# Kernel tuning notes

Measured on AMD Instinct MI355X. Metric: run time of the kernel, lower is better.

Reference implementation:

```python
import jax, jax.numpy as jnp
import numpy as np
from jax import lax

B, T_PAST, T_FUT, F_IN, F_OUT, H = 512, 128, 48, 64, 16, 512


def setup_inputs() -> dict:
    key = jax.random.key(0)
    ks = jax.random.split(key, 12)
    s = jnp.float32(0.05)
    p = lambda k, shape: jax.random.normal(k, shape, jnp.float32) * s
    return {
        "inp": jax.random.normal(ks[0], (B, T_PAST, F_IN), jnp.float32),
        "target_seq": jax.random.normal(ks[1], (B, T_FUT, F_OUT), jnp.float32),
        "enc1_Wk": p(ks[2], (F_IN, 4 * H)), "enc1_Wr": p(ks[3], (H, 4 * H)), "enc1_b": jnp.zeros((4 * H,), jnp.float32),
        "enc2_Wk": p(ks[4], (H, 4 * H)), "enc2_Wr": p(ks[5], (H, 4 * H)), "enc2_b": jnp.zeros((4 * H,), jnp.float32),
        "dec1_Wk": p(ks[6], (F_OUT, 4 * H)), "dec1_Wr": p(ks[7], (H, 4 * H)), "dec1_b": jnp.zeros((4 * H,), jnp.float32),
        "dec2_Wk": p(ks[8], (H, 4 * H)), "dec2_Wr": p(ks[9], (H, 4 * H)), "dec2_b": jnp.zeros((4 * H,), jnp.float32),
        "fc_W": p(ks[10], (H, F_OUT)), "fc_b": jnp.zeros((F_OUT,), jnp.float32),
    }


def _gates(z, c_prev):
    # Keras gate order: i, f, g(cell), o
    i, f, g, o = jnp.split(z, 4, axis=-1)
    c = jax.nn.sigmoid(f) * c_prev + jax.nn.sigmoid(i) * jnp.tanh(g)
    h = jax.nn.sigmoid(o) * jnp.tanh(c)
    return h, c


def _lstm_layer(xs, h0, c0, Wk, Wr, b):
    # xs: (B, T, D) -> (hs (B,T,H), hT, cT)
    xz = jnp.einsum("btd,dg->btg", xs, Wk) + b  # input projection precomputed
    def step(carry, xz_t):
        h, c = carry
        h2, c2 = _gates(xz_t + h @ Wr, c)
        return (h2, c2), h2
    (hT, cT), hs = lax.scan(step, (h0, c0), jnp.swapaxes(xz, 0, 1))
    return jnp.swapaxes(hs, 0, 1), hT, cT


def reference(inp, target_seq,
              enc1_Wk, enc1_Wr, enc1_b, enc2_Wk, enc2_Wr, enc2_b,
              dec1_Wk, dec1_Wr, dec1_b, dec2_Wk, dec2_Wr, dec2_b,
              fc_W, fc_b):
    b = inp.shape[0]
    z = jnp.zeros((b, H), inp.dtype)
    # Encoder: layer2 initial state = layer1 final state (as in source)
    h1s, h1, c1 = _lstm_layer(inp, z, z, enc1_Wk, enc1_Wr, enc1_b)
    _, h2, c2 = _lstm_layer(h1s, h1, c1, enc2_Wk, enc2_Wr, enc2_b)
    # Decoder: every future step restarts from (h2, c2) with teacher-forced
    # inputs -> steps are independent, compute all in parallel.
    z1 = (jnp.einsum("btf,fg->btg", target_seq, dec1_Wk)
          + (h2 @ dec1_Wr)[:, None, :] + dec1_b)          # (B, Tf, 4H)
    h1d, c1d = _gates(z1, c2[:, None, :])
    # layer2: input = h1d, initial state = (h1d, c1d) (chained per source)
    z2 = jnp.einsum("bth,hg->btg", h1d, dec2_Wk + dec2_Wr) + dec2_b
    h2d, _ = _gates(z2, c1d)
    return jnp.einsum("bth,hf->btf", h2d, fc_W) + fc_b    # (B, Tf, F_OUT)
```

## Files before the change

### kernel.cpp

```cpp
#include <hip/hip_runtime.h>


typedef _Float16 f16;
typedef _Float16 h8 __attribute__((ext_vector_type(8)));
typedef _Float16 h4 __attribute__((ext_vector_type(4)));
typedef float f32x4 __attribute__((ext_vector_type(4)));
typedef unsigned long long ull;

#define DEV static __device__ __forceinline__

constexpr int NB   = 512;
constexpr int TP   = 128;
constexpr int TFU  = 48;
constexpr int FIN  = 64;
constexpr int FOUT = 16;
constexpr int HS   = 512;
constexpr int G4   = 2048;

DEV float sigf(float x) { return 1.0f / (1.0f + __expf(-x)); }
DEV float tanh_(float x) { float e = __expf(2.0f * x); return 1.0f - 2.0f / (e + 1.0f); }

DEV void issue_ld(h8& d, const f16* p) {
  asm volatile("global_load_dwordx4 %0, %1, off" : "=v"(d) : "v"(p));
}
DEV void issue_ldc(h8& d, const f16* p) {
  asm volatile("global_load_dwordx4 %0, %1, off sc0 sc1" : "=v"(d) : "v"(p));
}
#define ILDX(dst, base, B) \
  asm volatile("global_load_dwordx4 %0, %1, off offset:" #B : "=v"(dst) : "v"(base));
#define ASM_VM0    asm volatile("s_waitcnt vmcnt(0)" ::: "memory")
#define ASM_VMC(N) asm volatile("s_waitcnt vmcnt(" #N ")" ::: "memory")
#define SBAR       __builtin_amdgcn_sched_barrier(0)

DEV void st_coh_h4(f16* p, h4 v) {
  union { h4 h; ull u; } c;
  c.h = v;
  __hip_atomic_store((ull*)p, c.u, __ATOMIC_RELAXED, __HIP_MEMORY_SCOPE_AGENT);
}

DEV unsigned xcc_id() {
  unsigned x;
  asm("s_getreg_b32 %0, hwreg(HW_REG_XCC_ID)" : "=s"(x));
  return x & 7;
}

DEV int ic2zc(int ic) { return ((ic >> 4) & 3) * 512 + ((ic >> 6) << 4) + (ic & 15); }

__global__ void k_conv(const float* __restrict__ a, const float* __restrict__ b,
                       f16* __restrict__ a16, f16* __restrict__ b16) {
  const size_t NA = (size_t)NB * TP * FIN;
  const size_t NBT = (size_t)NB * TFU * FOUT;
  for (size_t i = (size_t)blockIdx.x * blockDim.x + threadIdx.x; i < NA + NBT;
       i += (size_t)gridDim.x * blockDim.x) {
    if (i < NA) a16[i] = (f16)a[i];
    else        b16[i - NA] = (f16)b[i - NA];
  }
}

__global__ void k_bias(const float* __restrict__ b1, const float* __restrict__ b2,
                       const float* __restrict__ b3, const float* __restrict__ b4,
                       float* __restrict__ o1, float* __restrict__ o2,
                       float* __restrict__ o3, float* __restrict__ o4) {
  int ic = blockIdx.x * blockDim.x + threadIdx.x;
  if (ic < G4) {
    int zc = ic2zc(ic);
    o1[ic] = b1[zc]; o2[ic] = b2[zc]; o3[ic] = b3[zc]; o4[ic] = b4[zc];
  }
}

__global__ void k_pack(const float* __restrict__ A, const float* __restrict__ Bs,
                       int split, int NKC, int mode, f16* __restrict__ dst) {
  int i = blockIdx.x * blockDim.x + threadIdx.x;
  int total = 128 * NKC * 64;
  if (i >= total) return;
  int lane = i & 63, rem = i >> 6;
  int kc = rem % NKC, nt = rem / NKC;
  int zc = ic2zc(nt * 16 + (lane & 15));
  int k0 = kc * 32 + ((lane >> 4) << 3);
  h8 v;
#pragma unroll
  for (int j = 0; j < 8; j++) {
    int k = k0 + j;
    float x;
    if (mode == 2) x = A[(size_t)k * G4 + zc] + Bs[(size_t)k * G4 + zc];
    else x = (k < split) ? A[(size_t)k * G4 + zc] : Bs[(size_t)(k - split) * G4 + zc];
    v[j] = (f16)x;
  }
  *(h8*)(dst + (size_t)i * 8) = v;
}

__global__ void k_pack_dk16(const float* __restrict__ W, f16* __restrict__ dst) {
  int i = blockIdx.x * blockDim.x + threadIdx.x;
  if (i >= 128 * 64) return;
  int lane = i & 63, nt = i >> 6;
  int zc = ic2zc(nt * 16 + (lane & 15));
  h4 v;
#pragma unroll
  for (int j = 0; j < 4; j++) v[j] = (f16)W[(size_t)(((lane >> 4) << 2) + j) * G4 + zc];
  *(h4*)(dst + (size_t)i * 4) = v;
}

__global__ void k_pack_fc(const float* __restrict__ W, f16* __restrict__ dst) {
  int i = blockIdx.x * blockDim.x + threadIdx.x;
  if (i >= 32 * 64) return;
  int lane = i & 63, q = i >> 6;
  h4 v;
#pragma unroll
  for (int j = 0; j < 4; j++) {
    int k = q * 16 + ((lane >> 4) << 2) + j;
    v[j] = (f16)W[(size_t)k * FOUT + (lane & 15)];
  }
  *(h4*)(dst + (size_t)i * 4) = v;
}

template <int L, bool HIST>
__global__ __launch_bounds__(256, 1) void k_enc(
    const f16* __restrict__ wfrag, const float* __restrict__ biasI,
    f16* __restrict__ h1s, f16* __restrict__ h2r, f16* __restrict__ h2s,
    float* __restrict__ cT, const float* __restrict__ cInit,
    const f16* __restrict__ inp16, unsigned int* __restrict__ flags,
    int* __restrict__ roster) {
  constexpr int XKC = (L == 1) ? 2 : 16;
  constexpr int NKC = XKC + 16;
  constexpr size_t SLOT = (size_t)NB * HS;
  constexpr bool PLAIN_H = (L == 1) || HIST;

  extern __shared__ __align__(16) char smem[];
  f16* Bl = (f16*)smem;
  float* zl = (float*)(smem + (size_t)NKC * 4096);
  __shared__ int s_gc[2];

  const int tid = threadIdx.x, lane = tid & 63, wid = tid >> 6;
  const int wr = wid & 1, wc = wid >> 1;

  if (tid == 0) {
    unsigned x = xcc_id();
    int slot = atomicAdd(&roster[x], 1) & 31;
    s_gc[0] = (int)x; s_gc[1] = slot;
  }
  __syncthreads();
  const int g = s_gc[0], c = s_gc[1];
  const int b0 = g * 64;
  const int l15 = lane & 15, lk = (lane >> 4) << 3;
  const int trow = tid >> 2, tcol = (tid & 3) << 2;
  const int fbase = g * 32;

  const int kc0 = ((c >> 1) + 1) & 15;
  ull m1 = 0;
  for (int i = 0; i < 8; i++) m1 |= (3ull << (2 * ((kc0 + i) & 15)));
  const ull m2 = 0xFFFFFFFFull & ~m1;

  {
    const uint4* src = (const uint4*)wfrag + (size_t)c * NKC * 256;
    uint4* dst = (uint4*)smem;
    for (int i = tid; i < NKC * 256; i += 256) dst[i] = src[i];
  }

  float bs[4][4];
#pragma unroll
  for (int ga = 0; ga < 4; ga++) {
    f32x4 bv = *(const f32x4*)(biasI + 64 * c + 16 * ga + tcol);
#pragma unroll
    for (int jj = 0; jj < 4; jj++) bs[ga][jj] = bv[jj];
  }

  float cst[4];
  if (L == 1) {
    cst[0] = cst[1] = cst[2] = cst[3] = 0.0f;
  } else {
    f32x4 cv = *(const f32x4*)(cInit + (size_t)(b0 + trow) * HS + 16 * c + tcol);
#pragma unroll
    for (int jj = 0; jj < 4; jj++) cst[jj] = cv[jj];
  }

  int arow[2];
#pragma unroll
  for (int m = 0; m < 2; m++) arow[m] = b0 + 32 * wr + 16 * m + l15;

  const f16* bbase[2];
#pragma unroll
  for (int n = 0; n < 2; n++) bbase[n] = Bl + ((size_t)(2 * wc + n) * NKC * 64 + lane) * 8;
  const f16* bh0 = bbase[0] + (size_t)XKC * 512;
  const f16* bh1 = bbase[1] + (size_t)XKC * 512;

  const size_t aoff0 = ((size_t)(lk >> 4) * 512 + arow[0]) * 16 + (lk & 8);
  const size_t aoff1 = ((size_t)(lk >> 4) * 512 + arow[1]) * 16 + (lk & 8);

  __syncthreads();

#define POLLW(MASK)                                                            \
  {                                                                            \
    const unsigned int tgt = (unsigned int)t;                                  \
    for (;;) {                                                                 \
      unsigned int v = __hip_atomic_load(                                      \
          &flags[(size_t)(fbase + (lane & 31)) * 16], __ATOMIC_RELAXED,        \
          __HIP_MEMORY_SCOPE_AGENT);                                           \
      ull b = __ballot((int)(v >= tgt));                                       \
      if ((b & (MASK)) == (MASK)) break;                                       \
      __builtin_amdgcn_s_sleep(1);                                             \
    }                                                                          \
    SBAR;                                                                      \
  }

  for (int t = 0; t < TP; t++) {
    h8 ax0[XKC], ax1[XKC];
    if (L == 1) {
      const f16* xb0 = inp16 + ((size_t)arow[0] * TP + t) * FIN + lk;
      const f16* xb1 = inp16 + ((size_t)arow[1] * TP + t) * FIN + lk;
      ILDX(ax0[0], xb0, 0) ILDX(ax0[1], xb0, 64)
      ILDX(ax1[0], xb1, 0) ILDX(ax1[1], xb1, 64)
    } else {
      const f16* xb = h1s + (size_t)(t + 1) * SLOT;
      const f16* xp0 = xb + aoff0;
      const f16* xp1 = xb + aoff1;
#pragma unroll
      for (int kc = 0; kc < XKC; kc++) {
        issue_ld(ax0[kc], xp0);
        issue_ld(ax1[kc], xp1);
        xp0 += 16384; xp1 += 16384;
      }
    }

    if (t > 0) POLLW(m1);
    ASM_VM0; SBAR;

    const f16* hb;
    if (L == 1) hb = h1s + (size_t)t * SLOT;
    else if (HIST) hb = (t == 0) ? (h1s + (size_t)TP * SLOT) : (h2s + (size_t)(t - 1) * SLOT);
    else hb = (t == 0) ? (h1s + (size_t)TP * SLOT) : (h2r + (size_t)((t - 1) & 1) * SLOT);
    const f16* hpb0 = hb + aoff0;
    const f16* hpb1 = hb + aoff1;

    h8 hA0[4], hA1[4], hB0[4], hB1[4];
#define LD_H(D, P) { if constexpr (PLAIN_H) issue_ld(D, P); else issue_ldc(D, P); }
#define HB_ISSUE(B0, B1, P)                                                    \
  {                                                                            \
    _Pragma("unroll") for (int j = 0; j < 4; j++) {                            \
      int kk = (kc0 + (P) + j) & 15;                                           \
      const f16* q0 = hpb0 + (size_t)kk * 16384;                               \
      const f16* q1 = hpb1 + (size_t)kk * 16384;                               \
      LD_H(B0[j], q0)                                                          \
      LD_H(B1[j], q1)                                                          \
    }                                                                          \
  }
#define HB_MFMA(B0, B1, P)                                                     \
  {                                                                            \
    _Pragma("unroll") for (int j = 0; j < 4; j++) {                            \
      int kk = (kc0 + (P) + j) & 15;                                           \
      h8 bb0 = *(const h8*)(bh0 + (size_t)kk * 512);                           \
      h8 bb1 = *(const h8*)(bh1 + (size_t)kk * 512);                           \
      acc[0][0] = __builtin_amdgcn_mfma_f32_16x16x32_f16(B0[j], bb0, acc[0][0], 0, 0, 0); \
      acc[0][1] = __builtin_amdgcn_mfma_f32_16x16x32_f16(B0[j], bb1, acc[0][1], 0, 0, 0); \
      acc[1][0] = __builtin_amdgcn_mfma_f32_16x16x32_f16(B1[j], bb0, acc[1][0], 0, 0, 0); \
      acc[1][1] = __builtin_amdgcn_mfma_f32_16x16x32_f16(B1[j], bb1, acc[1][1], 0, 0, 0); \
    }                                                                          \
  }

    HB_ISSUE(hA0, hA1, 0)
    HB_ISSUE(hB0, hB1, 4)

    f32x4 acc[2][2] = {};

#pragma unroll
    for (int kc = 0; kc < XKC; kc++) {
      h8 bb0 = *(const h8*)(bbase[0] + (size_t)kc * 512);
      h8 bb1 = *(const h8*)(bbase[1] + (size_t)kc * 512);
      acc[0][0] = __builtin_amdgcn_mfma_f32_16x16x32_f16(ax0[kc], bb0, acc[0][0], 0, 0, 0);
      acc[0][1] = __builtin_amdgcn_mfma_f32_16x16x32_f16(ax0[kc], bb1, acc[0][1], 0, 0, 0);
      acc[1][0] = __builtin_amdgcn_mfma_f32_16x16x32_f16(ax1[kc], bb0, acc[1][0], 0, 0, 0);
      acc[1][1] = __builtin_amdgcn_mfma_f32_16x16x32_f16(ax1[kc], bb1, acc[1][1], 0, 0, 0);
    }

    ASM_VMC(8); SBAR;
    HB_MFMA(hA0, hA1, 0)
    if (t > 0) POLLW(m2);
    HB_ISSUE(hA0, hA1, 8)
    ASM_VMC(8); SBAR;
    HB_MFMA(hB0, hB1, 4)
    HB_ISSUE(hB0, hB1, 12)
    ASM_VMC(8); SBAR;
    HB_MFMA(hA0, hA1, 8)
    ASM_VMC(0); SBAR;
    HB_MFMA(hB0, hB1, 12)
#undef HB_ISSUE
#undef HB_MFMA
#undef LD_H

#pragma unroll
    for (int m = 0; m < 2; m++)
#pragma unroll
      for (int n = 0; n < 2; n++) {
        int zr = 32 * wr + 16 * m + ((lane >> 4) << 2);
        int zc_ = 32 * wc + 16 * n + l15;
#pragma unroll
        for (int r = 0; r < 4; r++) zl[(size_t)(zr + r) * 68 + zc_] = acc[m][n][r];
      }
    __syncthreads();

    h4 hv;
    {
      const float* zrow = zl + (size_t)trow * 68 + tcol;
      f32x4 z0 = *(const f32x4*)(zrow + 0);
      f32x4 z1 = *(const f32x4*)(zrow + 16);
      f32x4 z2 = *(const f32x4*)(zrow + 32);
      f32x4 z3 = *(const f32x4*)(zrow + 48);
#pragma unroll
      for (int jj = 0; jj < 4; jj++) {
        float zi = z0[jj] + bs[0][jj];
        float zf = z1[jj] + bs[1][jj];
        float zg = z2[jj] + bs[2][jj];
        float zo = z3[jj] + bs[3][jj];
        float ci = sigf(zf) * cst[jj] + sigf(zi) * tanh_(zg);
        cst[jj] = ci;
        hv[jj] = (f16)(sigf(zo) * tanh_(ci));
      }
    }
    {
      f16* hsl;
      if (L == 1) hsl = h1s + (size_t)(t + 1) * SLOT;
      else if (HIST) hsl = h2s + (size_t)t * SLOT;
      else hsl = h2r + (size_t)(t & 1) * SLOT;
      f16* hp = hsl + ((size_t)c * 512 + b0 + trow) * 16 + tcol;
      if constexpr (PLAIN_H) *(h4*)hp = hv;
      else st_coh_h4(hp, hv);
    }
    if (t == TP - 1) {
      f32x4 cp;
#pragma unroll
      for (int jj = 0; jj < 4; jj++) cp[jj] = cst[jj];
      *(f32x4*)(cT + (size_t)(b0 + trow) * HS + 16 * c + tcol) = cp;
    }

    ASM_VM0;
    __syncthreads();
    if (tid == 0)
      __hip_atomic_store(&flags[(size_t)(fbase + c) * 16], (unsigned int)(t + 1),
                         __ATOMIC_RELAXED, __HIP_MEMORY_SCOPE_AGENT);
  }
#undef POLLW
}

__global__ __launch_bounds__(256) void k_d1(const f16* __restrict__ h2T,
                                            const f16* __restrict__ wF,
                                            const float* __restrict__ bI,
                                            float* __restrict__ u) {
  const int tid = threadIdx.x, lane = tid & 63, wid = tid >> 6;
  const int wr = wid & 1, wc = wid >> 1;
  const int r0 = (blockIdx.x >> 4) * 32, ic0 = (blockIdx.x & 15) * 128;
  const int l15 = lane & 15, lk = (lane >> 4) << 3;
  const int arow = r0 + 16 * wr + l15;
  const f16* abase = h2T + ((size_t)(lk >> 4) * 512 + arow) * 16 + (lk & 8);
  const int nt0 = (ic0 >> 4) + 4 * wc;
  f32x4 acc[4] = {};
#pragma unroll
  for (int kc = 0; kc < 16; kc++) {
    h8 a = *(const h8*)(abase + (size_t)kc * 16384);
#pragma unroll
    for (int n = 0; n < 4; n++) {
      h8 b = *(const h8*)(wF + ((size_t)(nt0 + n) * 16 + kc) * 512 + (size_t)lane * 8);
      acc[n] = __builtin_amdgcn_mfma_f32_16x16x32_f16(a, b, acc[n], 0, 0, 0);
    }
  }
#pragma unroll
  for (int n = 0; n < 4; n++)
#pragma unroll
    for (int r = 0; r < 4; r++) {
      int row = r0 + 16 * wr + ((lane >> 4) << 2) + r;
      int ic = ic0 + 64 * wc + 16 * n + l15;
      u[(size_t)row * G4 + ic] = acc[n][r] + bI[ic];
    }
}

__global__ __launch_bounds__(256, 1) void k_d2(
    const f16* __restrict__ tg16, const f16* __restrict__ wk16F,
    const float* __restrict__ u, const float* __restrict__ c2T,
    const f16* __restrict__ w2F, const float* __restrict__ b2I,
    const f16* __restrict__ fcF, const float* __restrict__ fcb,
    float* __restrict__ out) {
  extern __shared__ __align__(16) char smem[];
  constexpr size_t H1OFF = 0;
  constexpr size_t C1OFF = 65536;
  constexpr size_t H2OFF = 131072;
  constexpr size_t RDOFF = 143360;

  const int tid = threadIdx.x, lane = tid & 63, wid = tid >> 6;
  const int l15 = lane & 15;
  const int r0 = blockIdx.x * 64;

  {
    const int wr = wid & 1, wc = wid >> 1;
    h4 a[2];
#pragma unroll
    for (int m = 0; m < 2; m++)
      a[m] = *(const h4*)(tg16 + (size_t)(r0 + 32 * wr + 16 * m + l15) * FOUT +
                          ((lane >> 4) << 2));
#pragma unroll 1
    for (int hc = 0; hc < 8; hc++) {
      f32x4 acc[2][8] = {};
#pragma unroll
      for (int n = 0; n < 8; n++) {
        int ntg = 16 * hc + 8 * wc + n;
        h4 b = *(const h4*)(wk16F + ((size_t)ntg * 64 + lane) * 4);
        acc[0][n] = __builtin_amdgcn_mfma_f32_16x16x16f16(a[0], b, acc[0][n], 0, 0, 0);
        acc[1][n] = __builtin_amdgcn_mfma_f32_16x16x16f16(a[1], b, acc[1][n], 0, 0, 0);
      }
#pragma unroll
      for (int m = 0; m < 2; m++)
#pragma unroll
        for (int s = 0; s < 2; s++) {
          int qq = 4 * hc + 2 * wc + s;
          int colh = 16 * qq + l15;
          int icb = 256 * hc + 128 * wc + 64 * s + l15;
#pragma unroll
          for (int r = 0; r < 4; r++) {
            int rl = 32 * wr + 16 * m + ((lane >> 4) << 2) + r;
            int grow = r0 + rl;
            int bidx = grow / 48;
            const float* ub = u + (size_t)bidx * G4;
            float zi = acc[m][4 * s + 0][r] + ub[icb];
            float zf = acc[m][4 * s + 1][r] + ub[icb + 16];
            float zg = acc[m][4 * s + 2][r] + ub[icb + 32];
            float zo = acc[m][4 * s + 3][r] + ub[icb + 48];
            float c2v = c2T[(size_t)bidx * HS + colh];
            float c1 = sigf(zf) * c2v + sigf(zi) * tanh_(zg);
            float h1 = sigf(zo) * tanh_(c1);
            size_t hb = (((size_t)rl * 1024) + (size_t)colh * 2) ^ (size_t)((rl & 7) << 4);
            *(f16*)(smem + H1OFF + hb) = (f16)h1;
            *(f16*)(smem + C1OFF + (size_t)rl * 1024 + (size_t)colh * 2) = (f16)c1;
          }
        }
    }
  }
  __syncthreads();

  {
    const int w = wid;
    f32x4 facc[4] = {};
#pragma unroll 1
    for (int sc = 0; sc < 8; sc++) {
      f32x4 acc[4][4] = {};
#pragma unroll
      for (int kc = 0; kc < 16; kc++) {
        h8 a[4];
#pragma unroll
        for (int mt = 0; mt < 4; mt++) {
          int rl = 16 * mt + l15;
          size_t ab = (((size_t)rl * 1024) + (size_t)(kc * 32 + ((lane >> 4) << 3)) * 2) ^
                      (size_t)((rl & 7) << 4);
          a[mt] = *(const h8*)(smem + H1OFF + ab);
        }
#pragma unroll
        for (int n = 0; n < 4; n++) {
          int nt = 32 * w + 4 * sc + n;
          h8 b = *(const h8*)(w2F + ((size_t)nt * 16 + kc) * 512 + (size_t)lane * 8);
#pragma unroll
          for (int mt = 0; mt < 4; mt++)
            acc[mt][n] = __builtin_amdgcn_mfma_f32_16x16x32_f16(a[mt], b, acc[mt][n], 0, 0, 0);
        }
      }
      int qq = 8 * w + sc;
#pragma unroll
      for (int mt = 0; mt < 4; mt++)
#pragma unroll
        for (int r = 0; r < 4; r++) {
          int rl = 16 * mt + ((lane >> 4) << 2) + r;
          int colh = 16 * qq + l15;
          int ic = 512 * w + 64 * sc + l15;
          float zi = acc[mt][0][r] + b2I[ic];
          float zf = acc[mt][1][r] + b2I[ic + 16];
          float zg = acc[mt][2][r] + b2I[ic + 32];
          float zo = acc[mt][3][r] + b2I[ic + 48];
          float c1v = (float)*(const f16*)(smem + C1OFF + (size_t)rl * 1024 + (size_t)colh * 2);
          float cn = sigf(zf) * c1v + sigf(zi) * tanh_(zg);
          float h2v = sigf(zo) * tanh_(cn);
          *(f16*)(smem + H2OFF + (size_t)w * 3072 + (size_t)rl * 48 + (size_t)l15 * 2) = (f16)h2v;
        }
#pragma unroll
      for (int mt = 0; mt < 4; mt++) {
        h4 aa = *(const h4*)(smem + H2OFF + (size_t)w * 3072 + (size_t)(16 * mt + l15) * 48 +
                             ((lane >> 4) << 3));
        h4 bb = *(const h4*)(fcF + ((size_t)qq * 64 + lane) * 4);
        facc[mt] = __builtin_amdgcn_mfma_f32_16x16x16f16(aa, bb, facc[mt], 0, 0, 0);
      }
    }
#pragma unroll
    for (int mt = 0; mt < 4; mt++)
#pragma unroll
      for (int r = 0; r < 4; r++) {
        int rl = 16 * mt + ((lane >> 4) << 2) + r;
        *(float*)(smem + RDOFF + ((size_t)w * 1152 + (size_t)rl * 18 + l15) * 4) = facc[mt][r];
      }
  }
  __syncthreads();

  {
    int rl = tid >> 2, c4 = (tid & 3) * 4;
    f32x4 o;
#pragma unroll
    for (int j = 0; j < 4; j++) {
      float s = 0.0f;
#pragma unroll
      for (int w = 0; w < 4; w++)
        s += *(const float*)(smem + RDOFF + ((size_t)w * 1152 + (size_t)rl * 18 + c4 + j) * 4);
      o[j] = s + fcb[c4 + j];
    }
    *(f32x4*)(out + (size_t)(r0 + rl) * FOUT + c4) = o;
  }
}

extern "C" void kernel_launch(void* const* d_in, const int* in_sizes, int n_in,
                              void* d_out, int out_size, void* d_ws, size_t ws_size,
                              hipStream_t stream) {
  const float* inp     = (const float*)d_in[0];
  const float* target  = (const float*)d_in[1];
  const float* e1Wk    = (const float*)d_in[2];
  const float* e1Wr    = (const float*)d_in[3];
  const float* e1b     = (const float*)d_in[4];
  const float* e2Wk    = (const float*)d_in[5];
  const float* e2Wr    = (const float*)d_in[6];
  const float* e2b     = (const float*)d_in[7];
  const float* d1Wk    = (const float*)d_in[8];
  const float* d1Wr    = (const float*)d_in[9];
  const float* d1b     = (const float*)d_in[10];
  const float* d2Wk    = (const float*)d_in[11];
  const float* d2Wr    = (const float*)d_in[12];
  const float* d2b     = (const float*)d_in[13];
  const float* fcW     = (const float*)d_in[14];
  const float* fcb     = (const float*)d_in[15];
  float* out = (float*)d_out;

  char* ws = (char*)d_ws;
  size_t off = 0;
  auto carve = [&](size_t bytes) { char* p = ws + off; off += bytes; return p; };
  f16*   inp16 = (f16*)carve((size_t)NB * TP * FIN * 2);
  f16*   tg16  = (f16*)carve((size_t)NB * TFU * FOUT * 2);
  f16*   h1s   = (f16*)carve((size_t)(TP + 1) * NB * HS * 2);
  f16*   h2r   = (f16*)carve((size_t)2 * NB * HS * 2);
  float* c1T   = (float*)carve((size_t)NB * HS * 4);
  float* c2T   = (float*)carve((size_t)NB * HS * 4);
  float* ubuf  = (float*)carve((size_t)NB * G4 * 4);
  f16*   Wc1F  = (f16*)carve((size_t)576 * G4 * 2);
  f16*   Wc2F  = (f16*)carve((size_t)1024 * G4 * 2);
  f16*   d1WrF = (f16*)carve((size_t)512 * G4 * 2);
  f16*   W2sF  = (f16*)carve((size_t)512 * G4 * 2);
  f16*   dk16F = (f16*)carve((size_t)16 * G4 * 2);
  f16*   fcWF  = (f16*)carve((size_t)512 * FOUT * 2);
  float* eB1I  = (float*)carve((size_t)G4 * 4);
  float* eB2I  = (float*)carve((size_t)G4 * 4);
  float* dB1I  = (float*)carve((size_t)G4 * 4);
  float* dB2I  = (float*)carve((size_t)G4 * 4);
  unsigned int* flags = (unsigned int*)carve(2 * 256 * 64);
  int*   roster = (int*)carve(256);
  const size_t H2S_BYTES = (size_t)TP * NB * HS * 2;
  bool hist = (ws_size >= off + H2S_BYTES);
  f16* h2s = hist ? (f16*)carve(H2S_BYTES) : nullptr;
  (void)n_in; (void)in_sizes; (void)out_size;

  constexpr int LDS_E1 = 18 * 4096 + 64 * 68 * 4;
  constexpr int LDS_E2 = 32 * 4096 + 64 * 68 * 4;
  constexpr int LDS_D2 = 143360 + 18432;
  {
    void (*p1)(const f16*, const float*, f16*, f16*, f16*, float*, const float*, const f16*,
               unsigned int*, int*) = k_enc<1, true>;
    void (*p2a)(const f16*, const float*, f16*, f16*, f16*, float*, const float*, const f16*,
                unsigned int*, int*) = k_enc<2, true>;
    void (*p2b)(const f16*, const float*, f16*, f16*, f16*, float*, const float*, const f16*,
                unsigned int*, int*) = k_enc<2, false>;
    hipFuncSetAttribute((const void*)p1, hipFuncAttributeMaxDynamicSharedMemorySize, LDS_E1);
    hipFuncSetAttribute((const void*)p2a, hipFuncAttributeMaxDynamicSharedMemorySize, LDS_E2);
    hipFuncSetAttribute((const void*)p2b, hipFuncAttributeMaxDynamicSharedMemorySize, LDS_E2);
    hipFuncSetAttribute((const void*)k_d2, hipFuncAttributeMaxDynamicSharedMemorySize, LDS_D2);
  }

  hipMemsetAsync(flags, 0, 2 * 256 * 64 + 256, stream);
  hipMemsetAsync(h1s, 0, (size_t)NB * HS * 2, stream);

  k_conv<<<4096, 256, 0, stream>>>(inp, target, inp16, tg16);
  k_bias<<<8, 256, 0, stream>>>(e1b, e2b, d1b, d2b, eB1I, eB2I, dB1I, dB2I);
  k_pack<<<576, 256, 0, stream>>>(e1Wk, e1Wr, 64, 18, 1, Wc1F);
  k_pack<<<1024, 256, 0, stream>>>(e2Wk, e2Wr, 512, 32, 1, Wc2F);
  k_pack<<<512, 256, 0, stream>>>(d1Wr, d1Wr, 512, 16, 1, d1WrF);
  k_pack<<<512, 256, 0, stream>>>(d2Wk, d2Wr, 0, 16, 2, W2sF);
  k_pack_dk16<<<32, 256, 0, stream>>>(d1Wk, dk16F);
  k_pack_fc<<<8, 256, 0, stream>>>(fcW, fcWF);

  k_enc<1, true><<<256, 256, LDS_E1, stream>>>(Wc1F, eB1I, h1s, h2r, h2s, c1T, nullptr,
                                               inp16, flags, roster);
  unsigned int* flags2 = flags + 256 * 16;
  int* roster2 = roster + 8;
  if (hist)
    k_enc<2, true><<<256, 256, LDS_E2, stream>>>(Wc2F, eB2I, h1s, h2r, h2s, c2T, c1T,
                                                 nullptr, flags2, roster2);
  else
    k_enc<2, false><<<256, 256, LDS_E2, stream>>>(Wc2F, eB2I, h1s, h2r, h2s, c2T, c1T,
                                                  nullptr, flags2, roster2);

  const f16* h2T = hist ? (h2s + (size_t)(TP - 1) * NB * HS) : (h2r + (size_t)1 * NB * HS);
  k_d1<<<256, 256, 0, stream>>>(h2T, d1WrF, dB1I, ubuf);
  k_d2<<<384, 256, LDS_D2, stream>>>(tg16, dk16F, ubuf, c2T, W2sF, dB2I, fcWF, fcb, out);
}
```

Before: 1.377 ms.

## Double encoder waves per block and replace per-block flags with per-step counters

```diff
diff --git a/kernel.cpp b/kernel.cpp
--- a/kernel.cpp
+++ b/kernel.cpp
@@ -4,7 +4,9 @@
 typedef _Float16 f16;
 typedef _Float16 h8 __attribute__((ext_vector_type(8)));
 typedef _Float16 h4 __attribute__((ext_vector_type(4)));
+typedef _Float16 h2v __attribute__((ext_vector_type(2)));
 typedef float f32x4 __attribute__((ext_vector_type(4)));
+typedef float f32x2 __attribute__((ext_vector_type(2)));
 typedef unsigned long long ull;
 
 #define DEV static __device__ __forceinline__
@@ -32,10 +34,10 @@
 #define ASM_VMC(N) asm volatile("s_waitcnt vmcnt(" #N ")" ::: "memory")
 #define SBAR       __builtin_amdgcn_sched_barrier(0)
 
-DEV void st_coh_h4(f16* p, h4 v) {
-  union { h4 h; ull u; } c;
+DEV void st_coh_h2(f16* p, h2v v) {
+  union { h2v h; unsigned u; } c;
   c.h = v;
-  __hip_atomic_store((ull*)p, c.u, __ATOMIC_RELAXED, __HIP_MEMORY_SCOPE_AGENT);
+  __hip_atomic_store((unsigned*)p, c.u, __ATOMIC_RELAXED, __HIP_MEMORY_SCOPE_AGENT);
 }
 
 DEV unsigned xcc_id() {
@@ -114,11 +116,11 @@
 }
 
 template <int L, bool HIST>
-__global__ __launch_bounds__(256, 1) void k_enc(
+__global__ __launch_bounds__(512, 2) void k_enc(
     const f16* __restrict__ wfrag, const float* __restrict__ biasI,
     f16* __restrict__ h1s, f16* __restrict__ h2r, f16* __restrict__ h2s,
     float* __restrict__ cT, const float* __restrict__ cInit,
-    const f16* __restrict__ inp16, unsigned int* __restrict__ flags,
+    const f16* __restrict__ inp16, unsigned int* __restrict__ cnt,
     int* __restrict__ roster) {
   constexpr int XKC = (L == 1) ? 2 : 16;
   constexpr int NKC = XKC + 16;
@@ -131,7 +133,7 @@
   __shared__ int s_gc[2];
 
   const int tid = threadIdx.x, lane = tid & 63, wid = tid >> 6;
-  const int wr = wid & 1, wc = wid >> 1;
+  const int wr4 = wid & 3, wc = wid >> 2;
 
   if (tid == 0) {
     unsigned x = xcc_id();
@@ -142,40 +144,32 @@
   const int g = s_gc[0], c = s_gc[1];
   const int b0 = g * 64;
   const int l15 = lane & 15, lk = (lane >> 4) << 3;
-  const int trow = tid >> 2, tcol = (tid & 3) << 2;
-  const int fbase = g * 32;
+  const int trow = tid >> 3, tcol = (tid & 7) << 1;
 
   const int kc0 = ((c >> 1) + 1) & 15;
-  ull m1 = 0;
-  for (int i = 0; i < 8; i++) m1 |= (3ull << (2 * ((kc0 + i) & 15)));
-  const ull m2 = 0xFFFFFFFFull & ~m1;
 
   {
     const uint4* src = (const uint4*)wfrag + (size_t)c * NKC * 256;
     uint4* dst = (uint4*)smem;
-    for (int i = tid; i < NKC * 256; i += 256) dst[i] = src[i];
-  }
-
-  float bs[4][4];
+    for (int i = tid; i < NKC * 256; i += 512) dst[i] = src[i];
+  }
+
+  float bs[4][2];
 #pragma unroll
   for (int ga = 0; ga < 4; ga++) {
-    f32x4 bv = *(const f32x4*)(biasI + 64 * c + 16 * ga + tcol);
-#pragma unroll
-    for (int jj = 0; jj < 4; jj++) bs[ga][jj] = bv[jj];
-  }
-
-  float cst[4];
+    f32x2 bv = *(const f32x2*)(biasI + 64 * c + 16 * ga + tcol);
+    bs[ga][0] = bv[0]; bs[ga][1] = bv[1];
+  }
+
+  float cst[2];
   if (L == 1) {
-    cst[0] = cst[1] = cst[2] = cst[3] = 0.0f;
+    cst[0] = cst[1] = 0.0f;
   } else {
-    f32x4 cv = *(const f32x4*)(cInit + (size_t)(b0 + trow) * HS + 16 * c + tcol);
-#pragma unroll
-    for (int jj = 0; jj < 4; jj++) cst[jj] = cv[jj];
-  }
-
-  int arow[2];
-#pragma unroll
-  for (int m = 0; m < 2; m++) arow[m] = b0 + 32 * wr + 16 * m + l15;
+    f32x2 cv = *(const f32x2*)(cInit + (size_t)(b0 + trow) * HS + 16 * c + tcol);
+    cst[0] = cv[0]; cst[1] = cv[1];
+  }
+
+  const int arow = b0 + 16 * wr4 + l15;
 
   const f16* bbase[2];
 #pragma unroll
@@ -183,129 +177,104 @@
   const f16* bh0 = bbase[0] + (size_t)XKC * 512;
   const f16* bh1 = bbase[1] + (size_t)XKC * 512;
 
-  const size_t aoff0 = ((size_t)(lk >> 4) * 512 + arow[0]) * 16 + (lk & 8);
-  const size_t aoff1 = ((size_t)(lk >> 4) * 512 + arow[1]) * 16 + (lk & 8);
+  const size_t aoff = ((size_t)(lk >> 4) * 512 + arow) * 16 + (lk & 8);
+
+  unsigned int* cbase = cnt + (size_t)g * TP * 16;
 
   __syncthreads();
 
-#define POLLW(MASK)                                                            \
-  {                                                                            \
-    const unsigned int tgt = (unsigned int)t;                                  \
-    for (;;) {                                                                 \
-      unsigned int v = __hip_atomic_load(                                      \
-          &flags[(size_t)(fbase + (lane & 31)) * 16], __ATOMIC_RELAXED,        \
-          __HIP_MEMORY_SCOPE_AGENT);                                           \
-      ull b = __ballot((int)(v >= tgt));                                       \
-      if ((b & (MASK)) == (MASK)) break;                                       \
-      __builtin_amdgcn_s_sleep(1);                                             \
-    }                                                                          \
-    SBAR;                                                                      \
-  }
-
   for (int t = 0; t < TP; t++) {
-    h8 ax0[XKC], ax1[XKC];
+    h8 ax[XKC];
     if (L == 1) {
-      const f16* xb0 = inp16 + ((size_t)arow[0] * TP + t) * FIN + lk;
-      const f16* xb1 = inp16 + ((size_t)arow[1] * TP + t) * FIN + lk;
-      ILDX(ax0[0], xb0, 0) ILDX(ax0[1], xb0, 64)
-      ILDX(ax1[0], xb1, 0) ILDX(ax1[1], xb1, 64)
+      const f16* xb = inp16 + ((size_t)arow * TP + t) * FIN + lk;
+      ILDX(ax[0], xb, 0) ILDX(ax[1], xb, 64)
     } else {
-      const f16* xb = h1s + (size_t)(t + 1) * SLOT;
-      const f16* xp0 = xb + aoff0;
-      const f16* xp1 = xb + aoff1;
+      const f16* xp = h1s + (size_t)(t + 1) * SLOT + aoff;
 #pragma unroll
       for (int kc = 0; kc < XKC; kc++) {
-        issue_ld(ax0[kc], xp0);
-        issue_ld(ax1[kc], xp1);
-        xp0 += 16384; xp1 += 16384;
+        issue_ld(ax[kc], xp);
+        xp += 16384;
       }
     }
-
-    if (t > 0) POLLW(m1);
     ASM_VM0; SBAR;
+
+    f32x4 acc[2] = {};
+#pragma unroll
+    for (int kc = 0; kc < XKC; kc++) {
+      h8 bb0 = *(const h8*)(bbase[0] + (size_t)kc * 512);
+      h8 bb1 = *(const h8*)(bbase[1] + (size_t)kc * 512);
+      acc[0] = __builtin_amdgcn_mfma_f32_16x16x32_f16(ax[kc], bb0, acc[0], 0, 0, 0);
+      acc[1] = __builtin_amdgcn_mfma_f32_16x16x32_f16(ax[kc], bb1, acc[1], 0, 0, 0);
+    }
+
+    if (t > 0) {
+      const unsigned int* cp = cbase + (size_t)(t - 1) * 16;
+      while (__hip_atomic_load(cp, __ATOMIC_RELAXED, __HIP_MEMORY_SCOPE_AGENT) < 32u)
+        __builtin_amdgcn_s_sleep(1);
+      SBAR;
+    }
 
     const f16* hb;
     if (L == 1) hb = h1s + (size_t)t * SLOT;
     else if (HIST) hb = (t == 0) ? (h1s + (size_t)TP * SLOT) : (h2s + (size_t)(t - 1) * SLOT);
     else hb = (t == 0) ? (h1s + (size_t)TP * SLOT) : (h2r + (size_t)((t - 1) & 1) * SLOT);
-    const f16* hpb0 = hb + aoff0;
-    const f16* hpb1 = hb + aoff1;
-
-    h8 hA0[4], hA1[4], hB0[4], hB1[4];
+    const f16* hpb = hb + aoff;
+
+    h8 hA[4], hB[4];
 #define LD_H(D, P) { if constexpr (PLAIN_H) issue_ld(D, P); else issue_ldc(D, P); }
-#define HB_ISSUE(B0, B1, P)                                                    \
+#define HB_ISSUE4(R, P)                                                        \
   {                                                                            \
     _Pragma("unroll") for (int j = 0; j < 4; j++) {                            \
       int kk = (kc0 + (P) + j) & 15;                                           \
-      const f16* q0 = hpb0 + (size_t)kk * 16384;                               \
-      const f16* q1 = hpb1 + (size_t)kk * 16384;                               \
-      LD_H(B0[j], q0)                                                          \
-      LD_H(B1[j], q1)                                                          \
+      const f16* q = hpb + (size_t)kk * 16384;                                 \
+      LD_H(R[j], q)                                                            \
     }                                                                          \
   }
-#define HB_MFMA(B0, B1, P)                                                     \
+#define HB_MFMA4(R, P)                                                         \
   {                                                                            \
     _Pragma("unroll") for (int j = 0; j < 4; j++) {                            \
       int kk = (kc0 + (P) + j) & 15;                                           \
       h8 bb0 = *(const h8*)(bh0 + (size_t)kk * 512);                           \
       h8 bb1 = *(const h8*)(bh1 + (size_t)kk * 512);                           \
-      acc[0][0] = __builtin_amdgcn_mfma_f32_16x16x32_f16(B0[j], bb0, acc[0][0], 0, 0, 0); \
-      acc[0][1] = __builtin_amdgcn_mfma_f32_16x16x32_f16(B0[j], bb1, acc[0][1], 0, 0, 0); \
-      acc[1][0] = __builtin_amdgcn_mfma_f32_16x16x32_f16(B1[j], bb0, acc[1][0], 0, 0, 0); \
-      acc[1][1] = __builtin_amdgcn_mfma_f32_16x16x32_f16(B1[j], bb1, acc[1][1], 0, 0, 0); \
+      acc[0] = __builtin_amdgcn_mfma_f32_16x16x32_f16(R[j], bb0, acc[0], 0, 0, 0); \
+      acc[1] = __builtin_amdgcn_mfma_f32_16x16x32_f16(R[j], bb1, acc[1], 0, 0, 0); \
     }                                                                          \
   }
 
-    HB_ISSUE(hA0, hA1, 0)
-    HB_ISSUE(hB0, hB1, 4)
-
-    f32x4 acc[2][2] = {};
-
-#pragma unroll
-    for (int kc = 0; kc < XKC; kc++) {
-      h8 bb0 = *(const h8*)(bbase[0] + (size_t)kc * 512);
-      h8 bb1 = *(const h8*)(bbase[1] + (size_t)kc * 512);
-      acc[0][0] = __builtin_amdgcn_mfma_f32_16x16x32_f16(ax0[kc], bb0, acc[0][0], 0, 0, 0);
-      acc[0][1] = __builtin_amdgcn_mfma_f32_16x16x32_f16(ax0[kc], bb1, acc[0][1], 0, 0, 0);
-      acc[1][0] = __builtin_amdgcn_mfma_f32_16x16x32_f16(ax1[kc], bb0, acc[1][0], 0, 0, 0);
-      acc[1][1] = __builtin_amdgcn_mfma_f32_16x16x32_f16(ax1[kc], bb1, acc[1][1], 0, 0, 0);
-    }
-
-    ASM_VMC(8); SBAR;
-    HB_MFMA(hA0, hA1, 0)
-    if (t > 0) POLLW(m2);
-    HB_ISSUE(hA0, hA1, 8)
-    ASM_VMC(8); SBAR;
-    HB_MFMA(hB0, hB1, 4)
-    HB_ISSUE(hB0, hB1, 12)
-    ASM_VMC(8); SBAR;
-    HB_MFMA(hA0, hA1, 8)
+    HB_ISSUE4(hA, 0)
+    HB_ISSUE4(hB, 4)
+    ASM_VMC(4); SBAR;
+    HB_MFMA4(hA, 0)
+    HB_ISSUE4(hA, 8)
+    ASM_VMC(4); SBAR;
+    HB_MFMA4(hB, 4)
+    HB_ISSUE4(hB, 12)
+    ASM_VMC(4); SBAR;
+    HB_MFMA4(hA, 8)
     ASM_VMC(0); SBAR;
-    HB_MFMA(hB0, hB1, 12)
-#undef HB_ISSUE
-#undef HB_MFMA
+    HB_MFMA4(hB, 12)
+#undef HB_ISSUE4
+#undef HB_MFMA4
 #undef LD_H
 
 #pragma unroll
-    for (int m = 0; m < 2; m++)
-#pragma unroll
-      for (int n = 0; n < 2; n++) {
-        int zr = 32 * wr + 16 * m + ((lane >> 4) << 2);
-        int zc_ = 32 * wc + 16 * n + l15;
-#pragma unroll
-        for (int r = 0; r < 4; r++) zl[(size_t)(zr + r) * 68 + zc_] = acc[m][n][r];
-      }
+    for (int n = 0; n < 2; n++) {
+      int zr = 16 * wr4 + ((lane >> 4) << 2);
+      int zc_ = 32 * wc + 16 * n + l15;
+#pragma unroll
+      for (int r = 0; r < 4; r++) zl[(size_t)(zr + r) * 68 + zc_] = acc[n][r];
+    }
     __syncthreads();
 
-    h4 hv;
+    h2v hv;
     {
       const float* zrow = zl + (size_t)trow * 68 + tcol;
-      f32x4 z0 = *(const f32x4*)(zrow + 0);
-      f32x4 z1 = *(const f32x4*)(zrow + 16);
-      f32x4 z2 = *(const f32x4*)(zrow + 32);
-      f32x4 z3 = *(const f32x4*)(zrow + 48);
-#pragma unroll
-      for (int jj = 0; jj < 4; jj++) {
+      f32x2 z0 = *(const f32x2*)(zrow + 0);
+      f32x2 z1 = *(const f32x2*)(zrow + 16);
+      f32x2 z2 = *(const f32x2*)(zrow + 32);
+      f32x2 z3 = *(const f32x2*)(zrow + 48);
+#pragma unroll
+      for (int jj = 0; jj < 2; jj++) {
         float zi = z0[jj] + bs[0][jj];
         float zf = z1[jj] + bs[1][jj];
         float zg = z2[jj] + bs[2][jj];
@@ -321,23 +290,21 @@
       else if (HIST) hsl = h2s + (size_t)t * SLOT;
       else hsl = h2r + (size_t)(t & 1) * SLOT;
       f16* hp = hsl + ((size_t)c * 512 + b0 + trow) * 16 + tcol;
-      if constexpr (PLAIN_H) *(h4*)hp = hv;
-      else st_coh_h4(hp, hv);
+      if constexpr (PLAIN_H) *(h2v*)hp = hv;
+      else st_coh_h2(hp, hv);
     }
     if (t == TP - 1) {
-      f32x4 cp;
-#pragma unroll
-      for (int jj = 0; jj < 4; jj++) cp[jj] = cst[jj];
-      *(f32x4*)(cT + (size_t)(b0 + trow) * HS + 16 * c + tcol) = cp;
+      f32x2 cp;
+      cp[0] = cst[0]; cp[1] = cst[1];
+      *(f32x2*)(cT + (size_t)(b0 + trow) * HS + 16 * c + tcol) = cp;
     }
 
     ASM_VM0;
     __syncthreads();
     if (tid == 0)
-      __hip_atomic_store(&flags[(size_t)(fbase + c) * 16], (unsigned int)(t + 1),
-                         __ATOMIC_RELAXED, __HIP_MEMORY_SCOPE_AGENT);
-  }
-#undef POLLW
+      __hip_atomic_fetch_add(cbase + (size_t)t * 16, 1u, __ATOMIC_RELAXED,
+                             __HIP_MEMORY_SCOPE_AGENT);
+  }
 }
 
 __global__ __launch_bounds__(256) void k_d1(const f16* __restrict__ h2T,
@@ -472,8 +439,8 @@
           float zo = acc[mt][3][r] + b2I[ic + 48];
           float c1v = (float)*(const f16*)(smem + C1OFF + (size_t)rl * 1024 + (size_t)colh * 2);
           float cn = sigf(zf) * c1v + sigf(zi) * tanh_(zg);
-          float h2v = sigf(zo) * tanh_(cn);
-          *(f16*)(smem + H2OFF + (size_t)w * 3072 + (size_t)rl * 48 + (size_t)l15 * 2) = (f16)h2v;
+          float h2v_ = sigf(zo) * tanh_(cn);
+          *(f16*)(smem + H2OFF + (size_t)w * 3072 + (size_t)rl * 48 + (size_t)l15 * 2) = (f16)h2v_;
         }
 #pragma unroll
       for (int mt = 0; mt < 4; mt++) {
@@ -549,7 +516,8 @@
   float* eB2I  = (float*)carve((size_t)G4 * 4);
   float* dB1I  = (float*)carve((size_t)G4 * 4);
   float* dB2I  = (float*)carve((size_t)G4 * 4);
-  unsigned int* flags = (unsigned int*)carve(2 * 256 * 64);
+  unsigned int* cnt1 = (unsigned int*)carve((size_t)8 * TP * 64);
+  unsigned int* cnt2 = (unsigned int*)carve((size_t)8 * TP * 64);
   int*   roster = (int*)carve(256);
   const size_t H2S_BYTES = (size_t)TP * NB * HS * 2;
   bool hist = (ws_size >= off + H2S_BYTES);
@@ -572,7 +540,7 @@
     hipFuncSetAttribute((const void*)k_d2, hipFuncAttributeMaxDynamicSharedMemorySize, LDS_D2);
   }
 
-  hipMemsetAsync(flags, 0, 2 * 256 * 64 + 256, stream);
+  hipMemsetAsync(cnt1, 0, (size_t)2 * 8 * TP * 64 + 256, stream);
   hipMemsetAsync(h1s, 0, (size_t)NB * HS * 2, stream);
 
   k_conv<<<4096, 256, 0, stream>>>(inp, target, inp16, tg16);
@@ -584,16 +552,15 @@
   k_pack_dk16<<<32, 256, 0, stream>>>(d1Wk, dk16F);
   k_pack_fc<<<8, 256, 0, stream>>>(fcW, fcWF);
 
-  k_enc<1, true><<<256, 256, LDS_E1, stream>>>(Wc1F, eB1I, h1s, h2r, h2s, c1T, nullptr,
-                                               inp16, flags, roster);
-  unsigned int* flags2 = flags + 256 * 16;
+  k_enc<1, true><<<256, 512, LDS_E1, stream>>>(Wc1F, eB1I, h1s, h2r, h2s, c1T, nullptr,
+                                               inp16, cnt1, roster);
   int* roster2 = roster + 8;
   if (hist)
-    k_enc<2, true><<<256, 256, LDS_E2, stream>>>(Wc2F, eB2I, h1s, h2r, h2s, c2T, c1T,
-                                                 nullptr, flags2, roster2);
+    k_enc<2, true><<<256, 512, LDS_E2, stream>>>(Wc2F, eB2I, h1s, h2r, h2s, c2T, c1T,
+                                                 nullptr, cnt2, roster2);
   else
-    k_enc<2, false><<<256, 256, LDS_E2, stream>>>(Wc2F, eB2I, h1s, h2r, h2s, c2T, c1T,
-                                                  nullptr, flags2, roster2);
+    k_enc<2, false><<<256, 512, LDS_E2, stream>>>(Wc2F, eB2I, h1s, h2r, h2s, c2T, c1T,
+                                                  nullptr, cnt2, roster2);
 
   const f16* h2T = hist ? (h2s + (size_t)(TP - 1) * NB * HS) : (h2r + (size_t)1 * NB * HS);
   k_d1<<<256, 256, 0, stream>>>(h2T, d1WrF, dB1I, ubuf);
```

Result: faster. 1.258 ms (median of 3 runs) (-8.6%).
